# Performance work log

Measured on AMD Instinct MI355X. Metric: run time of the kernel, lower is better.

## Reference

```python
import jax, jax.numpy as jnp
import numpy as np

# Dims: T=64 steps, B=8 batch, H=128 hidden, NH=4 heads, D=2*H=256 cell dim
T, B, H, NH = 64, 8, 128, 4
D = 2 * H
EPS = 1e-5


def _bn(v, scale, bias):
    # flax BatchNorm (training mode): stats over all axes except feature (-1)
    axes = tuple(range(v.ndim - 1))
    mu = v.mean(axes, keepdims=True)
    var = v.var(axes, keepdims=True)
    return (v - mu) * jax.lax.rsqrt(var + EPS) * scale + bias


def setup_inputs() -> dict:
    key = jax.random.key(0)
    ks = iter(jax.random.split(key, 48))
    r = lambda shape, s=0.02: (jax.random.normal(next(ks), shape, jnp.float32) * s)
    z = lambda shape: jnp.zeros(shape, jnp.float32)
    o = lambda shape: jnp.ones(shape, jnp.float32)
    inp = {
        "x": jax.random.normal(next(ks), (T, B, H), jnp.float32),
        # per-head mLSTMCell params (stacked over NH heads), flax Linear: y = x @ W + b
        "Wq": r((NH, D, D)), "bq": z((NH, D)),
        "Wk": r((NH, D, D)), "bk": z((NH, D)),
        "Wv": r((NH, D, D)), "bv": z((NH, D)),
        "conv_k": r((4, 1, NH), 0.2), "conv_b": z((NH,)),  # 1->NH channel conv == per-head 1->1 conv
        "Wi": r((NH, D)), "bi": r((NH,), 0.01),
        "Wf": r((NH, D)),
        "bf": jax.random.uniform(next(ks), (NH,), jnp.float32, 3.0, 6.0),
        "Wo": r((NH, D, D)), "bo": z((NH, D)),
        "Wskip": r((NH, D, D)), "bskip": z((NH, D)),
        # block params
        "bn1_s": o((H,)), "bn1_b": z((H,)),
        "bn2_s": o((D,)), "bn2_b": z((D,)),
        "Wup1": r((H, D)), "bup1": z((D,)),
        "Wup2": r((H, D)), "bup2": z((D,)),
        "Wpoll": r((NH * D, D)), "bpoll": z((D,)),
        "Wdown": r((D, H)), "bdown": z((H,)),
    }
    return inp


def reference(x, Wq, bq, Wk, bk, Wv, bv, conv_k, conv_b, Wi, bi, Wf, bf,
              Wo, bo, Wskip, bskip, bn1_s, bn1_b, bn2_s, bn2_b,
              Wup1, bup1, Wup2, bup2, Wpoll, bpoll, Wdown, bdown):
    nh, d, _ = Wq.shape
    b = x.shape[1]
    inv_sqrt_d = 1.0 / jnp.sqrt(jnp.float32(d))

    def step(carry, xt):
        c, n, m = carry  # c: [nh,b,d,d], n: [nh,b,d], m: [nh,b]
        u = _bn(xt, bn1_s, bn1_b)                      # [b,H]
        trig = jax.nn.silu(u @ Wup2 + bup2)            # [b,d]
        xin = u @ Wup1 + bup1                          # [b,d] mlstm input
        outg = jax.nn.sigmoid(jnp.einsum('bd,hde->hbe', xin, Wo) + bo[:, None, :])
        it = jnp.einsum('bd,hd->hb', xin, Wi) + bi[:, None]
        ft = jnp.einsum('bd,hd->hb', xin, Wf) + bf[:, None]
        m_new = jnp.maximum(ft + m, it)
        ig = jnp.exp(it - m_new)
        fg = jnp.exp(ft + m - m_new)
        # causal-ish depthwise conv over feature axis (flax Conv SAME, k=4)
        qk = jax.lax.conv_general_dilated(xin[..., None], conv_k, (1,), 'SAME',
                                          dimension_numbers=('NWC', 'WIO', 'NWC')) + conv_b
        qk = jax.nn.silu(jnp.transpose(qk, (2, 0, 1)))  # [nh,b,d]
        k = (jnp.einsum('hbd,hde->hbe', qk, Wk) + bk[:, None, :]) * inv_sqrt_d
        q = jnp.einsum('hbd,hde->hbe', qk, Wq) + bq[:, None, :]
        v = jnp.einsum('bd,hde->hbe', xin, Wv) + bv[:, None, :]
        c_new = fg[:, :, None, None] * c + jnp.einsum('hb,hbi,hbj->hbij', ig, v, k)
        n_new = fg[..., None] * n + ig[..., None] * k
        scaler = 1.0 / jnp.maximum(jnp.abs(jnp.einsum('hbi,hbi->hb', n_new, q)), 1.0)
        h = outg * jnp.einsum('hbik,hbk->hbi', c_new, q) * scaler[..., None]
        h = h + jnp.einsum('hbd,hde->hbe', qk, Wskip) + bskip[:, None, :]
        ho = _bn(h, bn2_s, bn2_b)                      # [nh,b,d]
        ho = jnp.transpose(ho, (1, 0, 2)).reshape(b, nh * d)
        ho = ho @ Wpoll + bpoll                        # [b,d]
        y = (ho * trig) @ Wdown + bdown + xt           # residual
        return (c_new, n_new, m_new), y

    c0 = jnp.zeros((nh, b, d, d), x.dtype)
    n0 = jnp.zeros((nh, b, d), x.dtype)
    m0 = jnp.zeros((nh, b), x.dtype)
    _, ys = jax.lax.scan(step, (c0, n0, m0), x)
    return ys
```

## Files before the change

kernel.cpp:

```cpp
#include <hip/hip_runtime.h>
#include <hip/hip_bf16.h>

#define T_ 64
#define B_ 8
#define H_ 128
#define NH_ 4
#define D_ 256
#define TB_ 512
#define EPS_ 1e-5f

typedef short bf16x8 __attribute__((ext_vector_type(8)));
typedef float f32x4 __attribute__((ext_vector_type(4)));

__device__ __forceinline__ float silu_(float x){ return x / (1.0f + __expf(-x)); }
__device__ __forceinline__ float sigm_(float x){ return 1.0f / (1.0f + __expf(-x)); }
__device__ __forceinline__ unsigned short tobf_(float f){
  unsigned u = __float_as_uint(f);
  u += 0x7FFF + ((u >> 16) & 1);
  return (unsigned short)(u >> 16);
}
__device__ __forceinline__ int afrag_(int m, int k){
  return (((m >> 4)*8 + (k >> 5))*64 + ((k >> 3)&3)*16 + (m & 15))*8 + (k & 7);
}
__device__ __forceinline__ int afrag1024_(int m, int k){
  return (((m >> 4)*32 + (k >> 5))*64 + ((k >> 3)&3)*16 + (m & 15))*8 + (k & 7);
}

__global__ __launch_bounds__(256) void k_prepup(
    const float* __restrict__ Wq, const float* __restrict__ Wk, const float* __restrict__ Ws,
    const float* __restrict__ Wv, const float* __restrict__ Wo,
    const float* __restrict__ Wup1, const float* __restrict__ Wup2,
    const float* __restrict__ Wp, const float* __restrict__ Wd,
    const float* __restrict__ x, const float* __restrict__ bn1s, const float* __restrict__ bn1b,
    const float* __restrict__ bup1, const float* __restrict__ bup2,
    const float* __restrict__ ck, const float* __restrict__ cb,
    const float* __restrict__ Wi, const float* __restrict__ bi,
    const float* __restrict__ Wf, const float* __restrict__ bfv,
    unsigned short* __restrict__ Wqt, unsigned short* __restrict__ Wkt,
    unsigned short* __restrict__ Wst, unsigned short* __restrict__ Wvt,
    unsigned short* __restrict__ Wot,
    unsigned short* __restrict__ Wpt, unsigned short* __restrict__ Wdt,
    unsigned short* __restrict__ xinb, unsigned short* __restrict__ qkb,
    float* __restrict__ trig, float* __restrict__ itb, float* __restrict__ ftb){
  __shared__ float xs[16][257];
  __shared__ unsigned short ubl[2048];
  int bid = blockIdx.x;
  int tid = threadIdx.x;
  if (bid < 64){
    int u = bid;
    int mat = u >> 5, rt = u & 31;
    {
      int tt = tid >> 7, hf = tid & 127;
      int t = rt*2 + tt;
      const float* xp = x + t*(B_*H_) + hf;
      float v0[8]; float mu = 0.f;
      #pragma unroll
      for (int b = 0; b < 8; b++){ v0[b] = xp[b*H_]; mu += v0[b]; }
      mu *= 0.125f;
      float var = 0.f;
      #pragma unroll
      for (int b = 0; b < 8; b++){ float dd = v0[b]-mu; var += dd*dd; }
      var *= 0.125f;
      float sc = (1.0f/sqrtf(var + EPS_)) * bn1s[hf];
      float bs = bn1b[hf];
      int kb = hf >> 5, j = hf & 7;
      int lanebase = ((hf >> 3)&3)*16 + tt*8;
      unsigned short* up = ubl + kb*512 + j;
      #pragma unroll
      for (int b = 0; b < 8; b++)
        up[(lanebase + b)*8] = tobf_((v0[b]-mu)*sc + bs);
    }
    __syncthreads();
    int w = tid >> 6, l = tid & 63, lm = l & 15, lq = l >> 4;
    const float* Wf32 = (mat == 0) ? Wup1 : Wup2;
    f32x4 acc[4];
    #pragma unroll
    for (int nt = 0; nt < 4; nt++) acc[nt] = (f32x4){0.f,0.f,0.f,0.f};
    #pragma unroll
    for (int kb = 0; kb < 4; kb++){
      bf16x8 a = *(const bf16x8*)(ubl + kb*512 + l*8);
      int k0 = kb*32 + lq*8;
      #pragma unroll
      for (int nt = 0; nt < 4; nt++){
        int n = (w*4 + nt)*16 + lm;
        const float* src = Wf32 + k0*D_ + n;
        bf16x8 bfr;
        #pragma unroll
        for (int j = 0; j < 8; j++) bfr[j] = (short)tobf_(src[j*D_]);
        acc[nt] = __builtin_amdgcn_mfma_f32_16x16x32_bf16(a, bfr, acc[nt], 0, 0, 0);
      }
    }
    const float* bias = (mat == 0) ? bup1 : bup2;
    #pragma unroll
    for (int nt = 0; nt < 4; nt++){
      #pragma unroll
      for (int r = 0; r < 4; r++){
        int m = lq*4 + r;
        int row = rt*16 + m;
        int e = w*64 + nt*16 + lm;
        float vv = acc[nt][r] + bias[e];
        if (mat == 1){
          trig[row*D_ + e] = silu_(vv);
        } else {
          xinb[afrag_(row, e)] = tobf_(vv);
          xs[m][e] = vv;
        }
      }
    }
    if (mat == 0){
      __syncthreads();
      int d = tid;
      #pragma unroll 4
      for (int m = 0; m < 16; m++){
        float x0  = xs[m][d];
        float xm1 = (d >= 1)   ? xs[m][d-1] : 0.f;
        float xp1 = (d <= 254) ? xs[m][d+1] : 0.f;
        float xp2 = (d <= 253) ? xs[m][d+2] : 0.f;
        int rowg = rt*16 + m;
        int fa = afrag_(rowg, d);
        #pragma unroll
        for (int h = 0; h < NH_; h++){
          float a2 = cb[h];
          a2 = fmaf(xm1, ck[0*NH_+h], a2);
          a2 = fmaf(x0,  ck[1*NH_+h], a2);
          a2 = fmaf(xp1, ck[2*NH_+h], a2);
          a2 = fmaf(xp2, ck[3*NH_+h], a2);
          qkb[h*(TB_*D_) + fa] = tobf_(silu_(a2));
        }
      }
      int dot = tid >> 2, l4 = tid & 3;
      int h = dot >> 4, m = dot & 15;
      float ai = 0.f, af = 0.f;
      const float* wi = Wi + h*D_;
      const float* wf = Wf + h*D_;
      #pragma unroll 8
      for (int jj = 0; jj < 64; jj++){
        int k = l4*64 + jj;
        float xv = xs[m][k];
        ai = fmaf(xv, wi[k], ai);
        af = fmaf(xv, wf[k], af);
      }
      ai += __shfl_down(ai, 1); af += __shfl_down(af, 1);
      ai += __shfl_down(ai, 2); af += __shfl_down(af, 2);
      if (l4 == 0){
        int rowg = rt*16 + m;
        int t = rowg >> 3, b = rowg & 7;
        itb[(h*B_ + b)*T_ + t] = ai + bi[h];
        ftb[(h*B_ + b)*T_ + t] = af + bfv[h];
      }
    }
  } else if (bid < 704){
    int u = bid - 64;
    int sub = u & 31;
    int h   = (u >> 5) & 3;
    int mat = u >> 7;
    const float* Win; unsigned short* Wout;
    switch (mat){
      case 0: Win = Wq; Wout = Wqt; break;
      case 1: Win = Wk; Wout = Wkt; break;
      case 2: Win = Ws; Wout = Wst; break;
      case 3: Win = Wv; Wout = Wvt; break;
      default: Win = Wo; Wout = Wot; break;
    }
    Win  += h * (D_*D_);
    Wout += h * (D_*D_);
    int gid = sub*256 + tid;
    int combo = gid >> 6;
    int l = gid & 63;
    int lm = l & 15, lq = l >> 4;
    int nt = combo >> 3, kb = combo & 7;
    int n = nt*16 + lm;
    int k0 = kb*32 + lq*8;
    bf16x8 v;
    #pragma unroll
    for (int j = 0; j < 8; j++) v[j] = (short)tobf_(Win[(k0+j)*D_ + n]);
    *(bf16x8*)(Wout + (combo*64 + l)*8) = v;
  } else if (bid < 832){
    int gid = (bid - 704)*256 + tid;
    int combo = gid >> 6;
    int l = gid & 63;
    int lm = l & 15, lq = l >> 4;
    int nt = combo >> 5, kb = combo & 31;
    int n = nt*16 + lm;
    int k0 = kb*32 + lq*8;
    bf16x8 v;
    #pragma unroll
    for (int j = 0; j < 8; j++) v[j] = (short)tobf_(Wp[(k0+j)*D_ + n]);
    *(bf16x8*)(Wpt + (combo*64 + l)*8) = v;
  } else {
    int gid = (bid - 832)*256 + tid;
    int combo = gid >> 6;
    int l = gid & 63;
    int lm = l & 15, lq = l >> 4;
    int nt = combo >> 3, kb = combo & 7;
    int n = nt*16 + lm;
    int k0 = kb*32 + lq*8;
    bf16x8 v;
    #pragma unroll
    for (int j = 0; j < 8; j++) v[j] = (short)tobf_(Wd[(k0+j)*H_ + n]);
    *(bf16x8*)(Wdt + (combo*64 + l)*8) = v;
  }
}

__global__ __launch_bounds__(256) void k_gemm5(
    const unsigned short* __restrict__ qkb, const unsigned short* __restrict__ xinb,
    const unsigned short* __restrict__ Wqt, const unsigned short* __restrict__ Wkt,
    const unsigned short* __restrict__ Wst, const unsigned short* __restrict__ Wvt,
    const unsigned short* __restrict__ Wot,
    const float* __restrict__ bq, const float* __restrict__ bk, const float* __restrict__ bsk,
    const float* __restrict__ bv, const float* __restrict__ bo,
    unsigned short* __restrict__ qob, unsigned short* __restrict__ kob,
    unsigned short* __restrict__ vot,
    float* __restrict__ hb, float* __restrict__ og){
  int bid = blockIdx.x;
  int rt  = bid & 15;
  int h   = (bid >> 4) & 3;
  int mat = bid >> 6;
  int tid = threadIdx.x;
  int w = tid >> 6, l = tid & 63;
  int lm = l & 15, lq = l >> 4;
  int r0 = rt * 32;
  const unsigned short* A = (mat < 3) ? (qkb + h*(TB_*D_)) : xinb;
  const unsigned short* Bt;
  const float* bias;
  switch (mat){
    case 0: Bt = Wqt; bias = bq;  break;
    case 1: Bt = Wkt; bias = bk;  break;
    case 2: Bt = Wst; bias = bsk; break;
    case 3: Bt = Wvt; bias = bv;  break;
    default: Bt = Wot; bias = bo; break;
  }
  Bt += h*(D_*D_);
  f32x4 acc[2][4];
  #pragma unroll
  for (int mt = 0; mt < 2; mt++)
    #pragma unroll
    for (int nt = 0; nt < 4; nt++) acc[mt][nt] = (f32x4){0.f,0.f,0.f,0.f};
  const unsigned short* Ap = A + l*8;
  const unsigned short* Bp = Bt + l*8;
  #pragma unroll
  for (int kc = 0; kc < 8; kc++){
    bf16x8 a0 = *(const bf16x8*)(Ap + ((rt*16      + kc) << 9));
    bf16x8 a1 = *(const bf16x8*)(Ap + ((rt*16 + 8  + kc) << 9));
    bf16x8 b0 = *(const bf16x8*)(Bp + (((w*4+0)*8 + kc) << 9));
    bf16x8 b1 = *(const bf16x8*)(Bp + (((w*4+1)*8 + kc) << 9));
    bf16x8 b2 = *(const bf16x8*)(Bp + (((w*4+2)*8 + kc) << 9));
    bf16x8 b3 = *(const bf16x8*)(Bp + (((w*4+3)*8 + kc) << 9));
    acc[0][0] = __builtin_amdgcn_mfma_f32_16x16x32_bf16(a0, b0, acc[0][0], 0, 0, 0);
    acc[0][1] = __builtin_amdgcn_mfma_f32_16x16x32_bf16(a0, b1, acc[0][1], 0, 0, 0);
    acc[0][2] = __builtin_amdgcn_mfma_f32_16x16x32_bf16(a0, b2, acc[0][2], 0, 0, 0);
    acc[0][3] = __builtin_amdgcn_mfma_f32_16x16x32_bf16(a0, b3, acc[0][3], 0, 0, 0);
    acc[1][0] = __builtin_amdgcn_mfma_f32_16x16x32_bf16(a1, b0, acc[1][0], 0, 0, 0);
    acc[1][1] = __builtin_amdgcn_mfma_f32_16x16x32_bf16(a1, b1, acc[1][1], 0, 0, 0);
    acc[1][2] = __builtin_amdgcn_mfma_f32_16x16x32_bf16(a1, b2, acc[1][2], 0, 0, 0);
    acc[1][3] = __builtin_amdgcn_mfma_f32_16x16x32_bf16(a1, b3, acc[1][3], 0, 0, 0);
  }
  float bval[4];
  #pragma unroll
  for (int nt = 0; nt < 4; nt++) bval[nt] = bias[h*D_ + w*64 + nt*16 + lm];
  #pragma unroll
  for (int mt = 0; mt < 2; mt++){
    #pragma unroll
    for (int r = 0; r < 4; r++){
      int row = r0 + mt*16 + lq*4 + r;
      int t = row >> 3, b = row & 7;
      #pragma unroll
      for (int nt = 0; nt < 4; nt++){
        int e = w*64 + nt*16 + lm;
        float vv = acc[mt][nt][r] + bval[nt];
        if (mat <= 1){
          if (mat == 1) vv *= 0.0625f;
          unsigned short* ob = (mat == 0) ? qob : kob;
          int mt2 = t >> 4, kb2 = e >> 5;
          int lane2 = ((e >> 3)&3)*16 + (t & 15);
          ob[(h*B_ + b)*16384 + ((mt2*8 + kb2)*64 + lane2)*8 + (e & 7)] = tobf_(vv);
        } else if (mat == 3){
          int nt3 = e >> 4, kb3 = t >> 5;
          int lane3 = ((t >> 3)&3)*16 + lm;
          vot[(h*B_ + b)*16384 + ((nt3*2 + kb3)*64 + lane3)*8 + (t & 7)] = tobf_(vv);
        } else {
          int obase = (((t*NH_ + h)*B_ + b) << 8) + e;
          if (mat == 4) og[obase] = sigm_(vv);
          else          hb[obase] = vv;
        }
      }
    }
  }
}

__global__ __launch_bounds__(256) void k_attn2(
    const unsigned short* __restrict__ qob, const unsigned short* __restrict__ kob,
    const unsigned short* __restrict__ vot, const float* __restrict__ og,
    const float* __restrict__ itb, const float* __restrict__ ftb,
    float* __restrict__ hb){
  __shared__ unsigned short Pf[1024];
  __shared__ float partial[4][16];
  __shared__ float scal[16];
  int bid = blockIdx.x;
  int hbx = bid >> 2, tq = bid & 3;
  int h = hbx >> 3, b = hbx & 7;
  int tid = threadIdx.x;
  int w = tid >> 6, l = tid & 63, lm = l & 15, lq = l >> 4;
  float F  = ftb[hbx*T_ + l];
  float it = itb[hbx*T_ + l];
  #pragma unroll
  for (int off = 1; off < 64; off <<= 1){
    float v2 = __shfl_up(F, off);
    if (l >= off) F += v2;
  }
  float ct = it - F;
  float G = ct;
  #pragma unroll
  for (int off = 1; off < 64; off <<= 1){
    float v2 = __shfl_up(G, off);
    if (l >= off) G = fmaxf(G, v2);
  }
  float rb = -fmaxf(0.f, G);
  const unsigned short* Aq = qob + hbx*16384 + l*8;
  const unsigned short* Bk = kob + hbx*16384 + l*8;
  f32x4 accs = (f32x4){0.f,0.f,0.f,0.f};
  #pragma unroll
  for (int kc = 0; kc < 8; kc++){
    bf16x8 a  = *(const bf16x8*)(Aq + ((tq*8 + kc) << 9));
    bf16x8 bb = *(const bf16x8*)(Bk + ((w*8  + kc) << 9));
    accs = __builtin_amdgcn_mfma_f32_16x16x32_bf16(a, bb, accs, 0, 0, 0);
  }
  int s = w*16 + lm;
  float ct_s = __shfl(ct, s);
  float p[4], ps[4];
  #pragma unroll
  for (int r = 0; r < 4; r++){
    int t = tq*16 + lq*4 + r;
    float rb_t = __shfl(rb, t);
    float pv = (s <= t) ? __expf(ct_s + rb_t) * accs[r] : 0.f;
    p[r] = pv; ps[r] = pv;
  }
  #pragma unroll
  for (int off = 1; off < 16; off <<= 1){
    #pragma unroll
    for (int r = 0; r < 4; r++) ps[r] += __shfl_xor(ps[r], off);
  }
  if (lm == 0){
    #pragma unroll
    for (int r = 0; r < 4; r++) partial[w][lq*4 + r] = ps[r];
  }
  {
    int kbP = w >> 1;
    int laneP = ((w*2 + (lm >> 3)) & 3)*16;
    int jP = lm & 7;
    #pragma unroll
    for (int r = 0; r < 4; r++){
      int m = lq*4 + r;
      Pf[(kbP*64 + laneP + m)*8 + jP] = tobf_(p[r]);
    }
  }
  __syncthreads();
  if (tid < 16){
    float sum = partial[0][tid] + partial[1][tid] + partial[2][tid] + partial[3][tid];
    scal[tid] = 1.0f / fmaxf(fabsf(sum), 1.0f);
  }
  bf16x8 pa0 = *(const bf16x8*)(Pf + l*8);
  bf16x8 pa1 = *(const bf16x8*)(Pf + 512 + l*8);
  const unsigned short* Bv = vot + hbx*16384 + l*8;
  f32x4 acco[4];
  #pragma unroll
  for (int nt = 0; nt < 4; nt++) acco[nt] = (f32x4){0.f,0.f,0.f,0.f};
  #pragma unroll
  for (int nt = 0; nt < 4; nt++){
    int nt3 = w*4 + nt;
    bf16x8 b0 = *(const bf16x8*)(Bv + (((nt3*2 + 0)) << 9));
    bf16x8 b1 = *(const bf16x8*)(Bv + (((nt3*2 + 1)) << 9));
    acco[nt] = __builtin_amdgcn_mfma_f32_16x16x32_bf16(pa0, b0, acco[nt], 0, 0, 0);
    acco[nt] = __builtin_amdgcn_mfma_f32_16x16x32_bf16(pa1, b1, acco[nt], 0, 0, 0);
  }
  __syncthreads();
  #pragma unroll
  for (int nt = 0; nt < 4; nt++){
    #pragma unroll
    for (int r = 0; r < 4; r++){
      int tl = lq*4 + r;
      int t = tq*16 + tl;
      int e = (w*4 + nt)*16 + lm;
      int idx = (((t*NH_ + h)*B_ + b) << 8) + e;
      hb[idx] += og[idx] * acco[nt][r] * scal[tl];
    }
  }
}

__global__ __launch_bounds__(256) void k_tail3(
    const float* __restrict__ hbuf, const float* __restrict__ bn2s, const float* __restrict__ bn2b,
    const unsigned short* __restrict__ Wpt, const float* __restrict__ bp,
    const float* __restrict__ trig, const unsigned short* __restrict__ Wdt,
    const float* __restrict__ bd, const float* __restrict__ x, float* __restrict__ y){
  __shared__ unsigned short hfr[16384];
  __shared__ unsigned short zf[4096];
  int u = blockIdx.x;
  int tid = threadIdx.x;
  int w = tid >> 6, l = tid & 63, lm = l & 15, lq = l >> 4;
  #pragma unroll
  for (int s = 0; s < 2; s++){
    int pair = tid + (s << 8);
    int tt = pair >> 8;
    int d  = pair & 255;
    int t  = u*2 + tt;
    const float* hp = hbuf + (t*NH_*B_)*D_ + d;
    float v[32]; float mu = 0.f;
    #pragma unroll
    for (int i = 0; i < 32; i++){ v[i] = hp[i*D_]; mu += v[i]; }
    mu *= (1.0f/32.0f);
    float var = 0.f;
    #pragma unroll
    for (int i = 0; i < 32; i++){ float dd = v[i]-mu; var += dd*dd; }
    var *= (1.0f/32.0f);
    float sc = (1.0f/sqrtf(var + EPS_)) * bn2s[d];
    float bs = bn2b[d];
    #pragma unroll
    for (int i = 0; i < 32; i++){
      int hh = i >> 3, b = i & 7;
      int m = tt*8 + b;
      int k = hh*D_ + d;
      hfr[afrag1024_(m, k)] = tobf_((v[i]-mu)*sc + bs);
    }
  }
  __syncthreads();
  f32x4 acc[4];
  #pragma unroll
  for (int nt = 0; nt < 4; nt++) acc[nt] = (f32x4){0.f,0.f,0.f,0.f};
  const unsigned short* Apl = hfr + l*8;
  const unsigned short* Bp  = Wpt + l*8;
  #pragma unroll 4
  for (int kc = 0; kc < 32; kc++){
    bf16x8 a = *(const bf16x8*)(Apl + (kc << 9));
    #pragma unroll
    for (int nt = 0; nt < 4; nt++){
      bf16x8 bfr = *(const bf16x8*)(Bp + ((((w*4+nt)*32) + kc) << 9));
      acc[nt] = __builtin_amdgcn_mfma_f32_16x16x32_bf16(a, bfr, acc[nt], 0, 0, 0);
    }
  }
  #pragma unroll
  for (int nt = 0; nt < 4; nt++){
    int e = w*64 + nt*16 + lm;
    float bpe = bp[e];
    #pragma unroll
    for (int r = 0; r < 4; r++){
      int ml = lq*4 + r;
      int row = u*16 + ml;
      float z = (acc[nt][r] + bpe) * trig[row*D_ + e];
      zf[afrag_(ml, e)] = tobf_(z);
    }
  }
  __syncthreads();
  f32x4 acc2[2];
  acc2[0] = (f32x4){0.f,0.f,0.f,0.f};
  acc2[1] = (f32x4){0.f,0.f,0.f,0.f};
  const unsigned short* Bdp = Wdt + l*8;
  #pragma unroll
  for (int kc = 0; kc < 8; kc++){
    bf16x8 a = *(const bf16x8*)(zf + (kc << 9) + l*8);
    #pragma unroll
    for (int q = 0; q < 2; q++){
      bf16x8 bb = *(const bf16x8*)(Bdp + (((w*2+q)*8 + kc) << 9));
      acc2[q] = __builtin_amdgcn_mfma_f32_16x16x32_bf16(a, bb, acc2[q], 0, 0, 0);
    }
  }
  #pragma unroll
  for (int q = 0; q < 2; q++){
    int hh = (w*2+q)*16 + lm;
    float bde = bd[hh];
    #pragma unroll
    for (int r = 0; r < 4; r++){
      int row = u*16 + lq*4 + r;
      y[row*H_ + hh] = acc2[q][r] + bde + x[row*H_ + hh];
    }
  }
}

extern "C" void kernel_launch(void* const* d_in, const int* in_sizes, int n_in,
                              void* d_out, int out_size, void* d_ws, size_t ws_size,
                              hipStream_t stream){
  const float* x     = (const float*)d_in[0];
  const float* Wq    = (const float*)d_in[1];
  const float* bq    = (const float*)d_in[2];
  const float* Wk    = (const float*)d_in[3];
  const float* bk    = (const float*)d_in[4];
  const float* Wv    = (const float*)d_in[5];
  const float* bv    = (const float*)d_in[6];
  const float* ck    = (const float*)d_in[7];
  const float* cb    = (const float*)d_in[8];
  const float* Wi    = (const float*)d_in[9];
  const float* bi    = (const float*)d_in[10];
  const float* Wf    = (const float*)d_in[11];
  const float* bf    = (const float*)d_in[12];
  const float* Wo    = (const float*)d_in[13];
  const float* bo    = (const float*)d_in[14];
  const float* Wsk   = (const float*)d_in[15];
  const float* bsk   = (const float*)d_in[16];
  const float* bn1s  = (const float*)d_in[17];
  const float* bn1b  = (const float*)d_in[18];
  const float* bn2s  = (const float*)d_in[19];
  const float* bn2b  = (const float*)d_in[20];
  const float* Wup1  = (const float*)d_in[21];
  const float* bup1  = (const float*)d_in[22];
  const float* Wup2  = (const float*)d_in[23];
  const float* bup2  = (const float*)d_in[24];
  const float* Wp    = (const float*)d_in[25];
  const float* bp    = (const float*)d_in[26];
  const float* Wd    = (const float*)d_in[27];
  const float* bd    = (const float*)d_in[28];
  float* y = (float*)d_out;

  float* w = (float*)d_ws;
  float* trig = w;  w += T_*B_*D_;
  float* hbuf = w;  w += T_*NH_*B_*D_;
  float* og   = w;  w += T_*NH_*B_*D_;
  float* itb  = w;  w += NH_*B_*T_;
  float* ftb  = w;  w += NH_*B_*T_;
  unsigned short* xinb = (unsigned short*)w;  w += (T_*B_*D_)/2;
  unsigned short* qkb  = (unsigned short*)w;  w += (NH_*TB_*D_)/2;
  unsigned short* Wqt  = (unsigned short*)w;  w += (NH_*D_*D_)/2;
  unsigned short* Wkt  = (unsigned short*)w;  w += (NH_*D_*D_)/2;
  unsigned short* Wst  = (unsigned short*)w;  w += (NH_*D_*D_)/2;
  unsigned short* Wvt  = (unsigned short*)w;  w += (NH_*D_*D_)/2;
  unsigned short* Wot  = (unsigned short*)w;  w += (NH_*D_*D_)/2;
  unsigned short* qob  = (unsigned short*)w;  w += (NH_*B_*T_*D_)/2;
  unsigned short* kob  = (unsigned short*)w;  w += (NH_*B_*T_*D_)/2;
  unsigned short* vot  = (unsigned short*)w;  w += (NH_*B_*T_*D_)/2;
  unsigned short* Wpt  = (unsigned short*)w;  w += (NH_*D_*D_)/2;
  unsigned short* Wdt  = (unsigned short*)w;  w += (D_*H_)/2;

  k_prepup<<<848, 256, 0, stream>>>(Wq, Wk, Wsk, Wv, Wo, Wup1, Wup2, Wp, Wd,
                                    x, bn1s, bn1b, bup1, bup2, ck, cb, Wi, bi, Wf, bf,
                                    Wqt, Wkt, Wst, Wvt, Wot, Wpt, Wdt,
                                    xinb, qkb, trig, itb, ftb);
  k_gemm5<<<320, 256, 0, stream>>>(qkb, xinb, Wqt, Wkt, Wst, Wvt, Wot,
                                   bq, bk, bsk, bv, bo, qob, kob, vot, hbuf, og);
  k_attn2<<<NH_*B_*4, 256, 0, stream>>>(qob, kob, vot, og, itb, ftb, hbuf);
  k_tail3<<<32, 256, 0, stream>>>(hbuf, bn2s, bn2b, Wpt, bp, trig, Wdt, bd, x, y);
}
```

Measured before the change: 155.3 us.

## Fuse gemm, attention and tail kernels into one persistent kernel with grid barriers

Merges the three post-prep kernels into a single 320-block kernel that runs the projection GEMM, chunked attention and tail phases in sequence. Software grid barriers built on an atomic counter (reset by the prep kernel) replace the kernel-launch boundaries, removing two launch gaps. The design relies on all 320 blocks being co-resident, which launch bounds of 2 blocks per CU are meant to ensure. If they are not all resident the barrier can deadlock, and blocks that have no work in the later phases still sit idle at the barriers.

```diff
diff --git a/kernel.cpp b/kernel.cpp
--- a/kernel.cpp
+++ b/kernel.cpp
@@ -8,6 +8,7 @@
 #define D_ 256
 #define TB_ 512
 #define EPS_ 1e-5f
+#define NBLK_B 320
 
 typedef short bf16x8 __attribute__((ext_vector_type(8)));
 typedef float f32x4 __attribute__((ext_vector_type(4)));
@@ -24,6 +25,18 @@
 }
 __device__ __forceinline__ int afrag1024_(int m, int k){
   return (((m >> 4)*32 + (k >> 5))*64 + ((k >> 3)&3)*16 + (m & 15))*8 + (k & 7);
+}
+
+__device__ __forceinline__ void gbar_(int* cnt, int target){
+  __syncthreads();
+  if (threadIdx.x == 0){
+    __threadfence();
+    __hip_atomic_fetch_add(cnt, 1, __ATOMIC_RELEASE, __HIP_MEMORY_SCOPE_AGENT);
+    while (__hip_atomic_load(cnt, __ATOMIC_ACQUIRE, __HIP_MEMORY_SCOPE_AGENT) < target)
+      __builtin_amdgcn_s_sleep(8);
+    __threadfence();
+  }
+  __syncthreads();
 }
 
 __global__ __launch_bounds__(256) void k_prepup(
@@ -41,11 +54,13 @@
     unsigned short* __restrict__ Wot,
     unsigned short* __restrict__ Wpt, unsigned short* __restrict__ Wdt,
     unsigned short* __restrict__ xinb, unsigned short* __restrict__ qkb,
-    float* __restrict__ trig, float* __restrict__ itb, float* __restrict__ ftb){
+    float* __restrict__ trig, float* __restrict__ itb, float* __restrict__ ftb,
+    int* __restrict__ cnt){
   __shared__ float xs[16][257];
   __shared__ unsigned short ubl[2048];
   int bid = blockIdx.x;
   int tid = threadIdx.x;
+  if (bid == 0 && tid == 0) *cnt = 0;
   if (bid < 64){
     int u = bid;
     int mat = u >> 5, rt = u & 31;
@@ -202,33 +217,32 @@
   }
 }
 
-__global__ __launch_bounds__(256) void k_gemm5(
-    const unsigned short* __restrict__ qkb, const unsigned short* __restrict__ xinb,
-    const unsigned short* __restrict__ Wqt, const unsigned short* __restrict__ Wkt,
-    const unsigned short* __restrict__ Wst, const unsigned short* __restrict__ Wvt,
-    const unsigned short* __restrict__ Wot,
-    const float* __restrict__ bq, const float* __restrict__ bk, const float* __restrict__ bsk,
-    const float* __restrict__ bv, const float* __restrict__ bo,
-    unsigned short* __restrict__ qob, unsigned short* __restrict__ kob,
-    unsigned short* __restrict__ vot,
-    float* __restrict__ hb, float* __restrict__ og){
-  int bid = blockIdx.x;
-  int rt  = bid & 15;
-  int h   = (bid >> 4) & 3;
-  int mat = bid >> 6;
-  int tid = threadIdx.x;
+struct KB {
+  const unsigned short *qkb, *xinb, *Wqt, *Wkt, *Wst, *Wvt, *Wot, *Wpt, *Wdt;
+  const float *bq, *bk, *bsk, *bv, *bo;
+  const float *itb, *ftb;
+  const float *bn2s, *bn2b, *bp, *trig, *bd, *x;
+  unsigned short *qob, *kob, *vot;
+  float *hbuf, *og, *y;
+  int* cnt;
+};
+
+__device__ __forceinline__ void ph_gemm5(const KB& p, int u, int tid){
+  int rt  = u & 15;
+  int h   = (u >> 4) & 3;
+  int mat = u >> 6;
   int w = tid >> 6, l = tid & 63;
   int lm = l & 15, lq = l >> 4;
   int r0 = rt * 32;
-  const unsigned short* A = (mat < 3) ? (qkb + h*(TB_*D_)) : xinb;
+  const unsigned short* A = (mat < 3) ? (p.qkb + h*(TB_*D_)) : p.xinb;
   const unsigned short* Bt;
   const float* bias;
   switch (mat){
-    case 0: Bt = Wqt; bias = bq;  break;
-    case 1: Bt = Wkt; bias = bk;  break;
-    case 2: Bt = Wst; bias = bsk; break;
-    case 3: Bt = Wvt; bias = bv;  break;
-    default: Bt = Wot; bias = bo; break;
+    case 0: Bt = p.Wqt; bias = p.bq;  break;
+    case 1: Bt = p.Wkt; bias = p.bk;  break;
+    case 2: Bt = p.Wst; bias = p.bsk; break;
+    case 3: Bt = p.Wvt; bias = p.bv;  break;
+    default: Bt = p.Wot; bias = p.bo; break;
   }
   Bt += h*(D_*D_);
   f32x4 acc[2][4];
@@ -270,39 +284,33 @@
         float vv = acc[mt][nt][r] + bval[nt];
         if (mat <= 1){
           if (mat == 1) vv *= 0.0625f;
-          unsigned short* ob = (mat == 0) ? qob : kob;
+          unsigned short* ob = (mat == 0) ? p.qob : p.kob;
           int mt2 = t >> 4, kb2 = e >> 5;
           int lane2 = ((e >> 3)&3)*16 + (t & 15);
           ob[(h*B_ + b)*16384 + ((mt2*8 + kb2)*64 + lane2)*8 + (e & 7)] = tobf_(vv);
         } else if (mat == 3){
           int nt3 = e >> 4, kb3 = t >> 5;
           int lane3 = ((t >> 3)&3)*16 + lm;
-          vot[(h*B_ + b)*16384 + ((nt3*2 + kb3)*64 + lane3)*8 + (t & 7)] = tobf_(vv);
+          p.vot[(h*B_ + b)*16384 + ((nt3*2 + kb3)*64 + lane3)*8 + (t & 7)] = tobf_(vv);
         } else {
           int obase = (((t*NH_ + h)*B_ + b) << 8) + e;
-          if (mat == 4) og[obase] = sigm_(vv);
-          else          hb[obase] = vv;
+          if (mat == 4) p.og[obase] = sigm_(vv);
+          else          p.hbuf[obase] = vv;
         }
       }
     }
   }
 }
 
-__global__ __launch_bounds__(256) void k_attn2(
-    const unsigned short* __restrict__ qob, const unsigned short* __restrict__ kob,
-    const unsigned short* __restrict__ vot, const float* __restrict__ og,
-    const float* __restrict__ itb, const float* __restrict__ ftb,
-    float* __restrict__ hb){
-  __shared__ unsigned short Pf[1024];
-  __shared__ float partial[4][16];
-  __shared__ float scal[16];
-  int bid = blockIdx.x;
-  int hbx = bid >> 2, tq = bid & 3;
+__device__ __forceinline__ void ph_attn(const KB& p, int u, int tid, unsigned char* smemraw){
+  unsigned short* Pf = (unsigned short*)smemraw;
+  float (*partial)[16] = (float (*)[16])(smemraw + 2048);
+  float* scal = (float*)(smemraw + 2048 + 256);
+  int hbx = u >> 2, tq = u & 3;
   int h = hbx >> 3, b = hbx & 7;
-  int tid = threadIdx.x;
   int w = tid >> 6, l = tid & 63, lm = l & 15, lq = l >> 4;
-  float F  = ftb[hbx*T_ + l];
-  float it = itb[hbx*T_ + l];
+  float F  = p.ftb[hbx*T_ + l];
+  float it = p.itb[hbx*T_ + l];
   #pragma unroll
   for (int off = 1; off < 64; off <<= 1){
     float v2 = __shfl_up(F, off);
@@ -316,8 +324,8 @@
     if (l >= off) G = fmaxf(G, v2);
   }
   float rb = -fmaxf(0.f, G);
-  const unsigned short* Aq = qob + hbx*16384 + l*8;
-  const unsigned short* Bk = kob + hbx*16384 + l*8;
+  const unsigned short* Aq = p.qob + hbx*16384 + l*8;
+  const unsigned short* Bk = p.kob + hbx*16384 + l*8;
   f32x4 accs = (f32x4){0.f,0.f,0.f,0.f};
   #pragma unroll
   for (int kc = 0; kc < 8; kc++){
@@ -327,13 +335,13 @@
   }
   int s = w*16 + lm;
   float ct_s = __shfl(ct, s);
-  float p[4], ps[4];
+  float pv4[4], ps[4];
   #pragma unroll
   for (int r = 0; r < 4; r++){
     int t = tq*16 + lq*4 + r;
     float rb_t = __shfl(rb, t);
     float pv = (s <= t) ? __expf(ct_s + rb_t) * accs[r] : 0.f;
-    p[r] = pv; ps[r] = pv;
+    pv4[r] = pv; ps[r] = pv;
   }
   #pragma unroll
   for (int off = 1; off < 16; off <<= 1){
@@ -351,7 +359,7 @@
     #pragma unroll
     for (int r = 0; r < 4; r++){
       int m = lq*4 + r;
-      Pf[(kbP*64 + laneP + m)*8 + jP] = tobf_(p[r]);
+      Pf[(kbP*64 + laneP + m)*8 + jP] = tobf_(pv4[r]);
     }
   }
   __syncthreads();
@@ -361,7 +369,7 @@
   }
   bf16x8 pa0 = *(const bf16x8*)(Pf + l*8);
   bf16x8 pa1 = *(const bf16x8*)(Pf + 512 + l*8);
-  const unsigned short* Bv = vot + hbx*16384 + l*8;
+  const unsigned short* Bv = p.vot + hbx*16384 + l*8;
   f32x4 acco[4];
   #pragma unroll
   for (int nt = 0; nt < 4; nt++) acco[nt] = (f32x4){0.f,0.f,0.f,0.f};
@@ -382,20 +390,14 @@
       int t = tq*16 + tl;
       int e = (w*4 + nt)*16 + lm;
       int idx = (((t*NH_ + h)*B_ + b) << 8) + e;
-      hb[idx] += og[idx] * acco[nt][r] * scal[tl];
-    }
-  }
-}
-
-__global__ __launch_bounds__(256) void k_tail3(
-    const float* __restrict__ hbuf, const float* __restrict__ bn2s, const float* __restrict__ bn2b,
-    const unsigned short* __restrict__ Wpt, const float* __restrict__ bp,
-    const float* __restrict__ trig, const unsigned short* __restrict__ Wdt,
-    const float* __restrict__ bd, const float* __restrict__ x, float* __restrict__ y){
-  __shared__ unsigned short hfr[16384];
-  __shared__ unsigned short zf[4096];
-  int u = blockIdx.x;
-  int tid = threadIdx.x;
+      p.hbuf[idx] += p.og[idx] * acco[nt][r] * scal[tl];
+    }
+  }
+}
+
+__device__ __forceinline__ void ph_tail(const KB& p, int u, int tid, unsigned char* smemraw){
+  unsigned short* hfr = (unsigned short*)smemraw;
+  unsigned short* zf  = (unsigned short*)(smemraw + 32768);
   int w = tid >> 6, l = tid & 63, lm = l & 15, lq = l >> 4;
   #pragma unroll
   for (int s = 0; s < 2; s++){
@@ -403,7 +405,7 @@
     int tt = pair >> 8;
     int d  = pair & 255;
     int t  = u*2 + tt;
-    const float* hp = hbuf + (t*NH_*B_)*D_ + d;
+    const float* hp = p.hbuf + (t*NH_*B_)*D_ + d;
     float v[32]; float mu = 0.f;
     #pragma unroll
     for (int i = 0; i < 32; i++){ v[i] = hp[i*D_]; mu += v[i]; }
@@ -412,8 +414,8 @@
     #pragma unroll
     for (int i = 0; i < 32; i++){ float dd = v[i]-mu; var += dd*dd; }
     var *= (1.0f/32.0f);
-    float sc = (1.0f/sqrtf(var + EPS_)) * bn2s[d];
-    float bs = bn2b[d];
+    float sc = (1.0f/sqrtf(var + EPS_)) * p.bn2s[d];
+    float bs = p.bn2b[d];
     #pragma unroll
     for (int i = 0; i < 32; i++){
       int hh = i >> 3, b = i & 7;
@@ -427,7 +429,7 @@
   #pragma unroll
   for (int nt = 0; nt < 4; nt++) acc[nt] = (f32x4){0.f,0.f,0.f,0.f};
   const unsigned short* Apl = hfr + l*8;
-  const unsigned short* Bp  = Wpt + l*8;
+  const unsigned short* Bp  = p.Wpt + l*8;
   #pragma unroll 4
   for (int kc = 0; kc < 32; kc++){
     bf16x8 a = *(const bf16x8*)(Apl + (kc << 9));
@@ -440,12 +442,12 @@
   #pragma unroll
   for (int nt = 0; nt < 4; nt++){
     int e = w*64 + nt*16 + lm;
-    float bpe = bp[e];
+    float bpe = p.bp[e];
     #pragma unroll
     for (int r = 0; r < 4; r++){
       int ml = lq*4 + r;
       int row = u*16 + ml;
-      float z = (acc[nt][r] + bpe) * trig[row*D_ + e];
+      float z = (acc[nt][r] + bpe) * p.trig[row*D_ + e];
       zf[afrag_(ml, e)] = tobf_(z);
     }
   }
@@ -453,7 +455,7 @@
   f32x4 acc2[2];
   acc2[0] = (f32x4){0.f,0.f,0.f,0.f};
   acc2[1] = (f32x4){0.f,0.f,0.f,0.f};
-  const unsigned short* Bdp = Wdt + l*8;
+  const unsigned short* Bdp = p.Wdt + l*8;
   #pragma unroll
   for (int kc = 0; kc < 8; kc++){
     bf16x8 a = *(const bf16x8*)(zf + (kc << 9) + l*8);
@@ -466,13 +468,24 @@
   #pragma unroll
   for (int q = 0; q < 2; q++){
     int hh = (w*2+q)*16 + lm;
-    float bde = bd[hh];
+    float bde = p.bd[hh];
     #pragma unroll
     for (int r = 0; r < 4; r++){
       int row = u*16 + lq*4 + r;
-      y[row*H_ + hh] = acc2[q][r] + bde + x[row*H_ + hh];
-    }
-  }
+      p.y[row*H_ + hh] = acc2[q][r] + bde + p.x[row*H_ + hh];
+    }
+  }
+}
+
+__global__ __launch_bounds__(256, 2) void k_body(KB p){
+  __shared__ alignas(16) unsigned char smem[40960];
+  int bid = blockIdx.x;
+  int tid = threadIdx.x;
+  ph_gemm5(p, bid, tid);
+  gbar_(p.cnt, NBLK_B);
+  if (bid < 128) ph_attn(p, bid, tid, smem);
+  gbar_(p.cnt, 2*NBLK_B);
+  if (bid < 32) ph_tail(p, bid, tid, smem);
 }
 
 extern "C" void kernel_launch(void* const* d_in, const int* in_sizes, int n_in,
@@ -527,13 +540,22 @@
   unsigned short* vot  = (unsigned short*)w;  w += (NH_*B_*T_*D_)/2;
   unsigned short* Wpt  = (unsigned short*)w;  w += (NH_*D_*D_)/2;
   unsigned short* Wdt  = (unsigned short*)w;  w += (D_*H_)/2;
+  int* cnt = (int*)w;
 
   k_prepup<<<848, 256, 0, stream>>>(Wq, Wk, Wsk, Wv, Wo, Wup1, Wup2, Wp, Wd,
                                     x, bn1s, bn1b, bup1, bup2, ck, cb, Wi, bi, Wf, bf,
                                     Wqt, Wkt, Wst, Wvt, Wot, Wpt, Wdt,
-                                    xinb, qkb, trig, itb, ftb);
-  k_gemm5<<<320, 256, 0, stream>>>(qkb, xinb, Wqt, Wkt, Wst, Wvt, Wot,
-                                   bq, bk, bsk, bv, bo, qob, kob, vot, hbuf, og);
-  k_attn2<<<NH_*B_*4, 256, 0, stream>>>(qob, kob, vot, og, itb, ftb, hbuf);
-  k_tail3<<<32, 256, 0, stream>>>(hbuf, bn2s, bn2b, Wpt, bp, trig, Wdt, bd, x, y);
-}
+                                    xinb, qkb, trig, itb, ftb, cnt);
+
+  KB P;
+  P.qkb = qkb; P.xinb = xinb; P.Wqt = Wqt; P.Wkt = Wkt; P.Wst = Wst; P.Wvt = Wvt;
+  P.Wot = Wot; P.Wpt = Wpt; P.Wdt = Wdt;
+  P.bq = bq; P.bk = bk; P.bsk = bsk; P.bv = bv; P.bo = bo;
+  P.itb = itb; P.ftb = ftb;
+  P.bn2s = bn2s; P.bn2b = bn2b; P.bp = bp; P.trig = trig; P.bd = bd; P.x = x;
+  P.qob = qob; P.kob = kob; P.vot = vot;
+  P.hbuf = hbuf; P.og = og; P.y = y;
+  P.cnt = cnt;
+
+  k_body<<<NBLK_B, 256, 0, stream>>>(P);
+}
```

Measured after the change: 265.9 us. 71.3% more time.
